# Kernel optimization log

Hardware: AMD Instinct MI355X
Metric: run time of the kernel (lower is better)

Reference implementation:

```python
import jax, jax.numpy as jnp
import numpy as np

PERTURBATION_SCALE = 0.01

def setup_inputs() -> dict:
    key = jax.random.key(0)
    k1, k2, k3 = jax.random.split(key, 3)
    theta = jax.random.normal(k1, (256, 512), dtype=jnp.float32)
    basis_eval = jax.random.normal(k2, (100000, 512), dtype=jnp.float32)
    noise = jax.random.normal(k3, (256, 512), dtype=jnp.float32)
    return {"theta": theta, "basis_eval": basis_eval, "noise": noise}

def reference(theta, basis_eval, noise):
    # phi: [N, K] functional evaluations
    phi_raw = basis_eval @ theta.T
    phi_perturbed = basis_eval @ (theta + noise * PERTURBATION_SCALE).T
    # sign-crossings between consecutive evaluation points: [N-1, K]
    crossings = (phi_raw[:-1] * phi_raw[1:] < 0).astype(theta.dtype)
    crossings_p = (phi_perturbed[:-1] * phi_perturbed[1:] < 0).astype(theta.dtype)
    persistence = crossings * crossings_p  # [N-1, K]
    # fused pairwise shared-persistence: Gram matrix [K, K]
    gram = persistence.T @ persistence
    K = theta.shape[0]
    iu, ju = jnp.triu_indices(K, k=1)  # row-major i<j == itertools.combinations order
    return gram[iu, ju]  # [K*(K-1)/2]
```

## Files before the change

kernel.cpp:

```cpp
#include <hip/hip_runtime.h>
#include <hip/hip_bf16.h>
#include <stdint.h>

#define KDIM    256
#define NWORDS  1564
#define NW      1563

typedef float  f32x4  __attribute__((ext_vector_type(4)));
typedef __bf16 bf16x8 __attribute__((ext_vector_type(8)));
typedef __bf16 bf16x4 __attribute__((ext_vector_type(4)));

__global__ void build_w(const float* __restrict__ theta,
                        const float* __restrict__ noise,
                        __bf16* __restrict__ Wt) {
    int idx = blockIdx.x * 256 + threadIdx.x;
    int j = idx >> 9;
    int d = idx & 511;
    float v;
    if (j < KDIM) v = theta[j * 512 + d];
    else          v = theta[(j - KDIM) * 512 + d] + 0.01f * noise[(j - KDIM) * 512 + d];
    Wt[((d >> 5) * 512 + j) * 32 + (d & 31)] = (__bf16)v;
}

__global__ void __launch_bounds__(512, 4)
gemm_signs(const float* __restrict__ basis,
           const __bf16* __restrict__ Wt,
           uint64_t* __restrict__ sbits) {
    __shared__ char smem[65536];

    const int tid    = threadIdx.x;
    const int lane   = tid & 63;
    const int wc     = tid >> 6;
    const int lane16 = lane & 15;
    const int lgrp   = lane >> 4;

    const int orig = blockIdx.x;
    const int x    = orig & 7;
    const int bm   = (x < 4 ? x * 196 : 784 + (x - 4) * 195) + (orig >> 3);

    const char* wbase = (const char*)Wt;
    int bfofs[4];
    #pragma unroll
    for (int n = 0; n < 4; ++n)
        bfofs[n] = (wc * 64 + n * 16 + lane16) * 64 + lgrp * 16;

    bf16x8 bf[2][4];
    #pragma unroll
    for (int n = 0; n < 4; ++n)
        bf[0][n] = *(const bf16x8*)(wbase + bfofs[n]);

    {
        const int rlo  = tid >> 7;
        const int cidx = (tid * 4) & 511;
        const int fg   = tid & 127;
        const int gsl  = fg >> 1;
        const int ghl  = (fg & 1) << 3;
        f32x4 ra[16];
        #pragma unroll
        for (int j = 0; j < 16; ++j) {
            int r = bm * 64 + j * 4 + rlo;
            if (r > 99999) r = 99999;
            ra[j] = *(const f32x4*)(basis + (size_t)r * 512 + cidx);
        }
        #pragma unroll
        for (int j = 0; j < 16; ++j) {
            const int row = j * 4 + rlo;
            bf16x4 v;
            v[0] = (__bf16)ra[j][0]; v[1] = (__bf16)ra[j][1];
            v[2] = (__bf16)ra[j][2]; v[3] = (__bf16)ra[j][3];
            *(bf16x4*)(smem + row * 1024 + ((gsl ^ row) << 4) + ghl) = v;
        }
    }
    __syncthreads();

    f32x4 acc[4][4] = {};
    #pragma unroll
    for (int t = 0; t < 16; ++t) {
        if (t < 15) {
            #pragma unroll
            for (int n = 0; n < 4; ++n)
                bf[(t + 1) & 1][n] =
                    *(const bf16x8*)(wbase + (size_t)(t + 1) * 32768 + bfofs[n]);
        }
        #pragma unroll
        for (int mh = 0; mh < 2; ++mh) {
            bf16x8 af[2];
            #pragma unroll
            for (int mi = 0; mi < 2; ++mi) {
                int rr = (mh * 2 + mi) * 16 + lane16;
                af[mi] = *(const bf16x8*)(smem + rr * 1024
                           + (((t * 4 + lgrp) ^ rr) << 4));
            }
            __builtin_amdgcn_s_setprio(1);
            #pragma unroll
            for (int mi = 0; mi < 2; ++mi)
                #pragma unroll
                for (int n = 0; n < 4; ++n)
                    acc[mh * 2 + mi][n] = __builtin_amdgcn_mfma_f32_16x16x32_bf16(
                        af[mi], bf[t & 1][n], acc[mh * 2 + mi][n], 0, 0, 0);
            __builtin_amdgcn_s_setprio(0);
        }
    }

    __syncthreads();
    unsigned char* sb = (unsigned char*)smem;
    #pragma unroll
    for (int m = 0; m < 4; ++m) {
        #pragma unroll
        for (int n = 0; n < 4; ++n) {
            int cc = wc * 64 + n * 16 + lane16;
            int rb = m * 16 + lgrp * 4;
            uint32_t pk = 0;
            #pragma unroll
            for (int rg = 0; rg < 4; ++rg)
                pk |= (acc[m][n][rg] < 0.0f ? 1u : 0u) << (8 * rg);
            *(uint32_t*)&sb[cc * 68 + rb] = pk;
        }
    }
    __syncthreads();

    {
        const unsigned char* src = &sb[tid * 68];
        uint64_t wbits = 0;
        #pragma unroll
        for (int k = 0; k < 16; ++k) {
            uint32_t qv = *(const uint32_t*)&src[4 * k];
            uint32_t p4 = ((qv & 0x01010101u) * 0x10204080u) >> 28;
            wbits |= (uint64_t)p4 << (4 * k);
        }
        sbits[(size_t)bm * 512 + tid] = wbits;
    }
}

__global__ void crossing_masks(const uint64_t* __restrict__ sbits,
                               uint64_t* __restrict__ maskT) {
    const int w = blockIdx.x;
    const int j = threadIdx.x;
    uint64_t s0r = sbits[(size_t)w * 512 + j];
    uint64_t s0p = sbits[(size_t)w * 512 + 256 + j];
    uint64_t s1r = sbits[(size_t)(w + 1) * 512 + j];
    uint64_t s1p = sbits[(size_t)(w + 1) * 512 + 256 + j];
    uint64_t cr = s0r ^ ((s0r >> 1) | (s1r << 63));
    uint64_t cp = s0p ^ ((s0p >> 1) | (s1p << 63));
    uint64_t m = cr & cp;
    if (w == NW - 1) m &= 0x7FFFFFFFull;
    maskT[(size_t)w * 256 + j] = m;
}

__global__ void zero_out(float* __restrict__ out) {
    int i = blockIdx.x * 256 + threadIdx.x;
    if (i < 32640) out[i] = 0.0f;
}

__global__ void pair_popcount(const uint64_t* __restrict__ maskT,
                              float* __restrict__ out) {
    const int i = blockIdx.x;
    const int c = blockIdx.y;
    const int j = threadIdx.x;
    if (j <= i) return;
    int w0 = c * 196;
    int w1 = w0 + 196; if (w1 > NW) w1 = NW;
    uint32_t sum = 0;
    #pragma unroll 4
    for (int w = w0; w < w1; ++w) {
        uint64_t mi = maskT[(size_t)w * 256 + i];
        uint64_t mj = maskT[(size_t)w * 256 + j];
        sum += (uint32_t)__popcll(mi & mj);
    }
    const size_t idx = (size_t)i * (2 * KDIM - i - 1) / 2 + (size_t)(j - i - 1);
    atomicAdd(&out[idx], (float)sum);
}

extern "C" void kernel_launch(void* const* d_in, const int* in_sizes, int n_in,
                              void* d_out, int out_size, void* d_ws, size_t ws_size,
                              hipStream_t stream) {
    const float* theta = (const float*)d_in[0];
    const float* basis = (const float*)d_in[1];
    const float* noise = (const float*)d_in[2];
    float* out = (float*)d_out;

    char* ws = (char*)d_ws;
    __bf16*   Wt    = (__bf16*)ws;
    uint64_t* sbits = (uint64_t*)(ws + 524288);
    uint64_t* maskT = (uint64_t*)(ws + 524288 + (size_t)NWORDS * 512 * 8);

    hipLaunchKernelGGL(build_w,        dim3(1024),    dim3(256), 0, stream, theta, noise, Wt);
    hipLaunchKernelGGL(gemm_signs,     dim3(NWORDS),  dim3(512), 0, stream, basis, Wt, sbits);
    hipLaunchKernelGGL(crossing_masks, dim3(NW),      dim3(256), 0, stream, sbits, maskT);
    hipLaunchKernelGGL(zero_out,       dim3(128),     dim3(256), 0, stream, out);
    hipLaunchKernelGGL(pair_popcount,  dim3(KDIM, 8), dim3(256), 0, stream, maskT, out);
}
```

Baseline: 129.9 us.

## Pre-cast basis to bf16 tiled layout in separate kernel, stream A fragments from global

Adds a cast_a kernel that converts the fp32 basis matrix to bf16 in a k-tiled layout written to workspace. The GEMM then loads A fragments directly from global memory into registers with a triple-buffered prefetch, instead of staging the tile through a 64KB LDS buffer. This removes the LDS staging and the barrier at the start of the GEMM and frees LDS for occupancy. The cost is an extra kernel launch and an extra round trip of about 100MB through HBM (write bf16, then read it back). It also drops the occupancy hint from the launch bounds.

After: 221.7 us. 1.71x slower.

```diff
diff --git a/kernel.cpp b/kernel.cpp
--- a/kernel.cpp
+++ b/kernel.cpp
@@ -5,6 +5,8 @@
 #define KDIM    256
 #define NWORDS  1564
 #define NW      1563
+#define AT_ROWS 100096
+#define AT_TSTRIDE ((size_t)AT_ROWS * 64)
 
 typedef float  f32x4  __attribute__((ext_vector_type(4)));
 typedef __bf16 bf16x8 __attribute__((ext_vector_type(8)));
@@ -22,11 +24,33 @@
     Wt[((d >> 5) * 512 + j) * 32 + (d & 31)] = (__bf16)v;
 }
 
-__global__ void __launch_bounds__(512, 4)
-gemm_signs(const float* __restrict__ basis,
+__global__ void __launch_bounds__(512)
+cast_a(const float* __restrict__ basis, __bf16* __restrict__ At) {
+    const int tid = threadIdx.x;
+    const int bm  = blockIdx.x;
+    const int rl  = tid >> 3;
+    const int oct = tid & 7;
+    int rsrc = bm * 64 + rl; if (rsrc > 99999) rsrc = 99999;
+    const float* src = basis + (size_t)rsrc * 512 + oct * 4;
+    const int rdst = bm * 64 + rl;
+
+    f32x4 v[16];
+    #pragma unroll
+    for (int t = 0; t < 16; ++t) v[t] = *(const f32x4*)(src + t * 32);
+    #pragma unroll
+    for (int t = 0; t < 16; ++t) {
+        bf16x4 o;
+        o[0] = (__bf16)v[t][0]; o[1] = (__bf16)v[t][1];
+        o[2] = (__bf16)v[t][2]; o[3] = (__bf16)v[t][3];
+        *(bf16x4*)((char*)At + (size_t)t * AT_TSTRIDE + (size_t)rdst * 64 + oct * 8) = o;
+    }
+}
+
+__global__ void __launch_bounds__(512)
+gemm_signs(const __bf16* __restrict__ At,
            const __bf16* __restrict__ Wt,
            uint64_t* __restrict__ sbits) {
-    __shared__ char smem[65536];
+    __shared__ unsigned char sb[512 * 68];
 
     const int tid    = threadIdx.x;
     const int lane   = tid & 63;
@@ -38,72 +62,51 @@
     const int x    = orig & 7;
     const int bm   = (x < 4 ? x * 196 : 784 + (x - 4) * 195) + (orig >> 3);
 
+    const char* abase = (const char*)At;
     const char* wbase = (const char*)Wt;
-    int bfofs[4];
+    int afofs[4], bfofs[4];
+    #pragma unroll
+    for (int m = 0; m < 4; ++m)
+        afofs[m] = (bm * 64 + m * 16 + lane16) * 64 + lgrp * 16;
     #pragma unroll
     for (int n = 0; n < 4; ++n)
         bfofs[n] = (wc * 64 + n * 16 + lane16) * 64 + lgrp * 16;
 
-    bf16x8 bf[2][4];
+    f32x4  acc[4][4] = {};
+    bf16x8 af[3][4], bf[3][4];
+
     #pragma unroll
-    for (int n = 0; n < 4; ++n)
-        bf[0][n] = *(const bf16x8*)(wbase + bfofs[n]);
+    for (int u = 0; u < 2; ++u) {
+        #pragma unroll
+        for (int m = 0; m < 4; ++m)
+            af[u][m] = *(const bf16x8*)(abase + (size_t)u * AT_TSTRIDE + afofs[m]);
+        #pragma unroll
+        for (int n = 0; n < 4; ++n)
+            bf[u][n] = *(const bf16x8*)(wbase + (size_t)u * 32768 + bfofs[n]);
+    }
 
-    {
-        const int rlo  = tid >> 7;
-        const int cidx = (tid * 4) & 511;
-        const int fg   = tid & 127;
-        const int gsl  = fg >> 1;
-        const int ghl  = (fg & 1) << 3;
-        f32x4 ra[16];
-        #pragma unroll
-        for (int j = 0; j < 16; ++j) {
-            int r = bm * 64 + j * 4 + rlo;
-            if (r > 99999) r = 99999;
-            ra[j] = *(const f32x4*)(basis + (size_t)r * 512 + cidx);
-        }
-        #pragma unroll
-        for (int j = 0; j < 16; ++j) {
-            const int row = j * 4 + rlo;
-            bf16x4 v;
-            v[0] = (__bf16)ra[j][0]; v[1] = (__bf16)ra[j][1];
-            v[2] = (__bf16)ra[j][2]; v[3] = (__bf16)ra[j][3];
-            *(bf16x4*)(smem + row * 1024 + ((gsl ^ row) << 4) + ghl) = v;
-        }
-    }
-    __syncthreads();
-
-    f32x4 acc[4][4] = {};
     #pragma unroll
     for (int t = 0; t < 16; ++t) {
-        if (t < 15) {
+        if (t < 14) {
+            const int nb = (t + 2) % 3;
+            #pragma unroll
+            for (int m = 0; m < 4; ++m)
+                af[nb][m] = *(const bf16x8*)(abase + (size_t)(t + 2) * AT_TSTRIDE + afofs[m]);
             #pragma unroll
             for (int n = 0; n < 4; ++n)
-                bf[(t + 1) & 1][n] =
-                    *(const bf16x8*)(wbase + (size_t)(t + 1) * 32768 + bfofs[n]);
+                bf[nb][n] = *(const bf16x8*)(wbase + (size_t)(t + 2) * 32768 + bfofs[n]);
         }
+        const int cb = t % 3;
+        __builtin_amdgcn_s_setprio(1);
         #pragma unroll
-        for (int mh = 0; mh < 2; ++mh) {
-            bf16x8 af[2];
+        for (int m = 0; m < 4; ++m)
             #pragma unroll
-            for (int mi = 0; mi < 2; ++mi) {
-                int rr = (mh * 2 + mi) * 16 + lane16;
-                af[mi] = *(const bf16x8*)(smem + rr * 1024
-                           + (((t * 4 + lgrp) ^ rr) << 4));
-            }
-            __builtin_amdgcn_s_setprio(1);
-            #pragma unroll
-            for (int mi = 0; mi < 2; ++mi)
-                #pragma unroll
-                for (int n = 0; n < 4; ++n)
-                    acc[mh * 2 + mi][n] = __builtin_amdgcn_mfma_f32_16x16x32_bf16(
-                        af[mi], bf[t & 1][n], acc[mh * 2 + mi][n], 0, 0, 0);
-            __builtin_amdgcn_s_setprio(0);
-        }
+            for (int n = 0; n < 4; ++n)
+                acc[m][n] = __builtin_amdgcn_mfma_f32_16x16x32_bf16(
+                    af[cb][m], bf[cb][n], acc[m][n], 0, 0, 0);
+        __builtin_amdgcn_s_setprio(0);
     }
 
-    __syncthreads();
-    unsigned char* sb = (unsigned char*)smem;
     #pragma unroll
     for (int m = 0; m < 4; ++m) {
         #pragma unroll
@@ -181,11 +184,13 @@
 
     char* ws = (char*)d_ws;
     __bf16*   Wt    = (__bf16*)ws;
-    uint64_t* sbits = (uint64_t*)(ws + 524288);
-    uint64_t* maskT = (uint64_t*)(ws + 524288 + (size_t)NWORDS * 512 * 8);
+    __bf16*   At    = (__bf16*)(ws + (1u << 20));
+    uint64_t* sbits = (uint64_t*)(ws + (110u << 20));
+    uint64_t* maskT = (uint64_t*)(ws + (118u << 20));
 
     hipLaunchKernelGGL(build_w,        dim3(1024),    dim3(256), 0, stream, theta, noise, Wt);
-    hipLaunchKernelGGL(gemm_signs,     dim3(NWORDS),  dim3(512), 0, stream, basis, Wt, sbits);
+    hipLaunchKernelGGL(cast_a,         dim3(NWORDS),  dim3(512), 0, stream, basis, At);
+    hipLaunchKernelGGL(gemm_signs,     dim3(NWORDS),  dim3(512), 0, stream, At, Wt, sbits);
     hipLaunchKernelGGL(crossing_masks, dim3(NW),      dim3(256), 0, stream, sbits, maskT);
     hipLaunchKernelGGL(zero_out,       dim3(128),     dim3(256), 0, stream, out);
     hipLaunchKernelGGL(pair_popcount,  dim3(KDIM, 8), dim3(256), 0, stream, maskT, out);
```
